# Kernel optimization log

Hardware: AMD Instinct MI355X
Metric: run time of the kernel (lower is better)

Reference implementation:

```python
import jax, jax.numpy as jnp
import numpy as np

NUM_HEADS = 16
KEY_SIZE = 64
D_MODEL = 1024


def setup_inputs() -> dict:
    key = jax.random.key(0)
    ks = jax.random.split(key, 9)
    B, S = 2, 2048
    HK = NUM_HEADS * KEY_SIZE
    s = 1.0 / np.sqrt(D_MODEL)
    return {
        "x": jax.random.normal(ks[0], (B, S, D_MODEL), dtype=jnp.float32),
        "Wq": jax.random.normal(ks[1], (D_MODEL, HK), dtype=jnp.float32) * s,
        "bq": jax.random.normal(ks[2], (HK,), dtype=jnp.float32) * 0.02,
        "Wk": jax.random.normal(ks[3], (D_MODEL, HK), dtype=jnp.float32) * s,
        "bk": jax.random.normal(ks[4], (HK,), dtype=jnp.float32) * 0.02,
        "Wv": jax.random.normal(ks[5], (D_MODEL, HK), dtype=jnp.float32) * s,
        "bv": jax.random.normal(ks[6], (HK,), dtype=jnp.float32) * 0.02,
        "Wo": jax.random.normal(ks[7], (HK, D_MODEL), dtype=jnp.float32) * s,
        "bo": jax.random.normal(ks[8], (D_MODEL,), dtype=jnp.float32) * 0.02,
    }


def reference(x, Wq, bq, Wk, bk, Wv, bv, Wo, bo):
    B, S, _ = x.shape
    H, K = NUM_HEADS, KEY_SIZE
    # QKV projections -> (B, H, S, K)
    def proj(W, b):
        return (x @ W + b).reshape(B, S, H, K).transpose(0, 2, 1, 3)
    q = proj(Wq, bq)
    k = proj(Wk, bk)
    v = proj(Wv, bv)
    scale = jnp.sqrt(jnp.float32(K))
    scores = jnp.einsum('bhsk,bhtk->bhst', q, k) / scale  # (B,H,S,S)
    attn = jax.nn.softmax(scores, axis=-1)
    out = jnp.einsum('bhst,bhtk->bhsk', attn, v)  # (B,H,S,K)
    out = out.transpose(0, 2, 1, 3).reshape(B, S, H * K)
    return out @ Wo + bo
```

## Files before the change

kernel.cpp:

```cpp
#include <hip/hip_runtime.h>


#define NH 16
#define KS 64
#define DM 1024
#define BB 2
#define SS 2048
#define NT (BB*SS)
#define HKD 1024
#define L2E 1.44269504088896340736f

typedef __attribute__((ext_vector_type(4))) float floatx4;
typedef __attribute__((ext_vector_type(8))) short short8;

__device__ __forceinline__ unsigned short f2b(float f) {
  unsigned u = __builtin_bit_cast(unsigned, f);
  u = (u + 0x7fffu + ((u >> 16) & 1u)) >> 16;
  return (unsigned short)u;
}

__device__ __forceinline__ floatx4 mfma16(short8 a, short8 b, floatx4 c) {
  return __builtin_amdgcn_mfma_f32_16x16x32_bf16(a, b, c, 0, 0, 0);
}

__device__ __forceinline__ void async16(const void* g, void* l) {
  __builtin_amdgcn_global_load_lds(
      (const __attribute__((address_space(1))) unsigned int*)g,
      (__attribute__((address_space(3))) unsigned int*)l, 16, 0, 0);
}

__global__ void cast_x_kernel(const float* __restrict__ x, unsigned short* __restrict__ xb) {
  int i = (blockIdx.x * 256 + threadIdx.x) * 4;
  float4 v = *(const float4*)(x + i);
  ushort4 o;
  o.x = f2b(v.x); o.y = f2b(v.y); o.z = f2b(v.z); o.w = f2b(v.w);
  *(ushort4*)(xb + i) = o;
}

__global__ void transw_kernel(const float* __restrict__ Wq, const float* __restrict__ Wk,
                              const float* __restrict__ Wv, const float* __restrict__ Wo,
                              unsigned short* __restrict__ wqt, unsigned short* __restrict__ wkt,
                              unsigned short* __restrict__ wvt, unsigned short* __restrict__ wot) {
  const float* W; unsigned short* Wt;
  if (blockIdx.z == 0)      { W = Wq; Wt = wqt; }
  else if (blockIdx.z == 1) { W = Wk; Wt = wkt; }
  else if (blockIdx.z == 2) { W = Wv; Wt = wvt; }
  else                      { W = Wo; Wt = wot; }
  __shared__ __align__(16) unsigned short tile[64][80];
  int k0 = blockIdx.x * 64, n0 = blockIdx.y * 64;
  int t = threadIdx.x;
  int c0 = (t & 15) * 4, r = t >> 4;
  #pragma unroll
  for (int p = 0; p < 4; ++p) {
    int rr = r + p * 16;
    float4 v = *(const float4*)(W + (k0 + rr) * DM + n0 + c0);
    tile[c0 + 0][rr] = f2b(v.x);
    tile[c0 + 1][rr] = f2b(v.y);
    tile[c0 + 2][rr] = f2b(v.z);
    tile[c0 + 3][rr] = f2b(v.w);
  }
  __syncthreads();
  int cc0 = (t & 7) * 8, rn = t >> 3;
  #pragma unroll
  for (int p = 0; p < 2; ++p) {
    int nn = rn + p * 32;
    *(short8*)(Wt + (n0 + nn) * DM + k0 + cc0) = *(const short8*)(&tile[nn][cc0]);
  }
}

__global__ __launch_bounds__(256) void gemm_qkv_kernel(
    const unsigned short* __restrict__ xb,
    const unsigned short* __restrict__ wqt, const unsigned short* __restrict__ wkt,
    const unsigned short* __restrict__ wvt,
    const float* __restrict__ bq, const float* __restrict__ bk, const float* __restrict__ bv,
    unsigned short* __restrict__ qb, unsigned short* __restrict__ kbuf,
    unsigned short* __restrict__ vbuf) {
  __shared__ __align__(16) unsigned short As[8192], Bs[8192];
  const unsigned short* Bt; const float* bias; unsigned short* dst; float scale;
  if (blockIdx.z == 0)      { Bt = wqt; bias = bq; dst = qb;   scale = 0.125f * L2E; }
  else if (blockIdx.z == 1) { Bt = wkt; bias = bk; dst = kbuf; scale = 1.0f; }
  else                      { Bt = wvt; bias = bv; dst = vbuf; scale = 1.0f; }
  int m0 = blockIdx.x * 128, n0 = blockIdx.y * 128;
  int t = threadIdx.x, w = t >> 6, lane = t & 63, cl = lane & 15, quad = lane >> 4;
  int clm = cl & 7;
  int wr = (w >> 1) * 64, wc = (w & 1) * 64;
  floatx4 acc[4][4];
  #pragma unroll
  for (int i = 0; i < 4; ++i)
    #pragma unroll
    for (int j = 0; j < 4; ++j)
      acc[i][j] = floatx4{0.f, 0.f, 0.f, 0.f};

  for (int kc = 0; kc < DM / 64; ++kc) {
    __syncthreads();
    #pragma unroll
    for (int i = 0; i < 4; ++i) {
      int c = i * 256 + t;
      int row = c >> 3, col8 = (c & 7) ^ (row & 7);
      async16(xb + (m0 + row) * DM + kc * 64 + col8 * 8, &As[c * 8]);
      async16(Bt + (n0 + row) * DM + kc * 64 + col8 * 8, &Bs[c * 8]);
    }
    asm volatile("s_waitcnt vmcnt(0)" ::: "memory");
    __syncthreads();
    #pragma unroll
    for (int kk = 0; kk < 2; ++kk) {
      short8 a[4], b[4];
      #pragma unroll
      for (int i = 0; i < 4; ++i)
        a[i] = *(const short8*)&As[(wr + i * 16 + cl) * 64 + (((kk * 4 + quad) ^ clm) * 8)];
      #pragma unroll
      for (int j = 0; j < 4; ++j)
        b[j] = *(const short8*)&Bs[(wc + j * 16 + cl) * 64 + (((kk * 4 + quad) ^ clm) * 8)];
      #pragma unroll
      for (int i = 0; i < 4; ++i)
        #pragma unroll
        for (int j = 0; j < 4; ++j)
          acc[i][j] = mfma16(a[i], b[j], acc[i][j]);
    }
  }
  int h = (n0 + wc) >> 6;
  #pragma unroll
  for (int j = 0; j < 4; ++j) {
    float bj = bias[n0 + wc + j * 16 + cl];
    int kd = j * 16 + cl;
    #pragma unroll
    for (int i = 0; i < 4; ++i)
      #pragma unroll
      for (int r = 0; r < 4; ++r) {
        int token = m0 + wr + i * 16 + quad * 4 + r;
        int bz = token >> 11, s = token & (SS - 1);
        float val = (acc[i][j][r] + bj) * scale;
        dst[(((bz * NH + h) * SS + s) << 6) + kd] = f2b(val);
      }
  }
}

__global__ void transv_kernel(const unsigned short* __restrict__ v,
                              unsigned short* __restrict__ vt) {
  __shared__ __align__(16) unsigned short tile[64][80];
  int s0 = blockIdx.x * 64, bh = blockIdx.y;
  int t = threadIdx.x;
  int kd0 = (t & 7) * 8, sl = t >> 3;
  #pragma unroll
  for (int p = 0; p < 2; ++p) {
    int sr = sl + p * 32;
    short8 vv = *(const short8*)(v + (bh * SS + s0 + sr) * KS + kd0);
    #pragma unroll
    for (int q = 0; q < 8; ++q) tile[kd0 + q][sr] = ((unsigned short*)&vv)[q];
  }
  __syncthreads();
  int sc0 = (t & 7) * 8, kl = t >> 3;
  #pragma unroll
  for (int p = 0; p < 2; ++p) {
    int kk = kl + p * 32;
    *(short8*)(vt + (bh * KS + kk) * SS + s0 + sc0) = *(const short8*)(&tile[kk][sc0]);
  }
}

__global__ __launch_bounds__(256) void attn_kernel(
    const unsigned short* __restrict__ Q, const unsigned short* __restrict__ Kb,
    const unsigned short* __restrict__ Vt, unsigned short* __restrict__ AO) {
  __shared__ __align__(16) unsigned short Ks[2][4096], Vs[2][4096];
  __shared__ __align__(16) unsigned short Ps[4][1024];
  int t = threadIdx.x, w = t >> 6, lane = t & 63, cl = lane & 15, quad = lane >> 4;
  int clm = cl & 7;
  int h = blockIdx.y, bz = blockIdx.z, bh = bz * NH + h;
  int q0 = blockIdx.x * 64 + w * 16;
  const unsigned short* Qp = Q + (bh * SS + q0) * KS;
  const unsigned short* Kp = Kb + bh * SS * KS;
  const unsigned short* Vp = Vt + bh * KS * SS;
  unsigned short* p_w = Ps[w];

  short8 qa[2];
  #pragma unroll
  for (int c = 0; c < 2; ++c)
    qa[c] = *(const short8*)(Qp + cl * KS + c * 32 + quad * 8);

  float l = 0.f;
  floatx4 oa[4];
  #pragma unroll
  for (int j = 0; j < 4; ++j) oa[j] = floatx4{0.f, 0.f, 0.f, 0.f};

  auto stage = [&](int tile, int buf) {
    const unsigned short* kp = Kp + (tile * 64) * KS;
    #pragma unroll
    for (int i = 0; i < 2; ++i) {
      int c = i * 256 + t;
      int row = c >> 3, col8 = (c & 7) ^ (row & 7);
      async16(kp + row * KS + col8 * 8, &Ks[buf][c * 8]);
    }
    #pragma unroll
    for (int i = 0; i < 2; ++i) {
      int c = i * 256 + t;
      int d = c >> 3, col8 = (c & 7) ^ (d & 7);
      async16(Vp + d * SS + tile * 64 + col8 * 8, &Vs[buf][c * 8]);
    }
  };
  stage(0, 0);
  stage(1, 1);

  const int NTILES = SS / 64;
  for (int it = 0; it < NTILES; ++it) {
    int cur = it & 1;
    if (it < NTILES - 1) asm volatile("s_waitcnt vmcnt(4)" ::: "memory");
    else                 asm volatile("s_waitcnt vmcnt(0)" ::: "memory");
    __syncthreads();

    floatx4 s[4];
    #pragma unroll
    for (int kt = 0; kt < 4; ++kt) {
      short8 kb0 = *(const short8*)&Ks[cur][(kt * 16 + cl) * 64 + ((quad ^ clm) * 8)];
      short8 kb1 = *(const short8*)&Ks[cur][(kt * 16 + cl) * 64 + (((4 + quad) ^ clm) * 8)];
      floatx4 z = {0.f, 0.f, 0.f, 0.f};
      s[kt] = mfma16(kb1, qa[1], mfma16(kb0, qa[0], z));
    }
    #pragma unroll
    for (int kt = 0; kt < 4; ++kt) {
      unsigned u[4];
      #pragma unroll
      for (int r = 0; r < 4; ++r) {
        float p = __builtin_amdgcn_exp2f(s[kt][r]);
        u[r] = __builtin_bit_cast(unsigned, p) & 0xffff0000u;
        l += __builtin_bit_cast(float, u[r]);
      }
      uint2 pk;
      pk.x = (u[0] >> 16) | u[1];
      pk.y = (u[2] >> 16) | u[3];
      int off = cl * 64 + (((kt * 2 + (quad >> 1)) ^ clm) * 8) + (quad & 1) * 4;
      *(uint2*)(p_w + off) = pk;
    }
    asm volatile("s_waitcnt lgkmcnt(0)" ::: "memory");
    short8 pa[2];
    #pragma unroll
    for (int c = 0; c < 2; ++c)
      pa[c] = *(const short8*)(p_w + cl * 64 + (((c * 4 + quad) ^ clm) * 8));
    #pragma unroll
    for (int j = 0; j < 4; ++j) {
      short8 vb0 = *(const short8*)&Vs[cur][(j * 16 + cl) * 64 + ((quad ^ clm) * 8)];
      short8 vb1 = *(const short8*)&Vs[cur][(j * 16 + cl) * 64 + (((4 + quad) ^ clm) * 8)];
      oa[j] = mfma16(vb1, pa[1], mfma16(vb0, pa[0], oa[j]));
    }
    __syncthreads();
    if (it + 2 < NTILES) stage(it + 2, cur);
  }

  l += __shfl_xor(l, 16);
  l += __shfl_xor(l, 32);
  float inv = 1.0f / l;
  unsigned short* aop = AO + (bz * SS + q0 + cl) * DM + h * KS + quad * 4;
  #pragma unroll
  for (int j = 0; j < 4; ++j) {
    unsigned short b0 = f2b(oa[j][0] * inv), b1 = f2b(oa[j][1] * inv);
    unsigned short b2 = f2b(oa[j][2] * inv), b3 = f2b(oa[j][3] * inv);
    uint2 pk;
    pk.x = (unsigned)b0 | ((unsigned)b1 << 16);
    pk.y = (unsigned)b2 | ((unsigned)b3 << 16);
    *(uint2*)(aop + j * 16) = pk;
  }
}

__global__ __launch_bounds__(128) void gemm_out_kernel(
    const unsigned short* __restrict__ ao, const unsigned short* __restrict__ wot,
    const float* __restrict__ bo, float* __restrict__ out) {
  __shared__ __align__(16) unsigned short As[8192], Bs[4096];
  int m0 = blockIdx.x * 128, n0 = blockIdx.y * 64;
  int t = threadIdx.x, w = t >> 6, lane = t & 63, cl = lane & 15, quad = lane >> 4;
  int clm = cl & 7;
  int wr = w * 64;
  floatx4 acc[4][4];
  #pragma unroll
  for (int i = 0; i < 4; ++i)
    #pragma unroll
    for (int j = 0; j < 4; ++j)
      acc[i][j] = floatx4{0.f, 0.f, 0.f, 0.f};

  for (int kc = 0; kc < HKD / 64; ++kc) {
    __syncthreads();
    #pragma unroll
    for (int i = 0; i < 8; ++i) {
      int c = i * 128 + t;
      int row = c >> 3, col8 = (c & 7) ^ (row & 7);
      async16(ao + (m0 + row) * HKD + kc * 64 + col8 * 8, &As[c * 8]);
    }
    #pragma unroll
    for (int i = 0; i < 4; ++i) {
      int c = i * 128 + t;
      int row = c >> 3, col8 = (c & 7) ^ (row & 7);
      async16(wot + (n0 + row) * HKD + kc * 64 + col8 * 8, &Bs[c * 8]);
    }
    asm volatile("s_waitcnt vmcnt(0)" ::: "memory");
    __syncthreads();
    #pragma unroll
    for (int kk = 0; kk < 2; ++kk) {
      short8 a[4], b[4];
      #pragma unroll
      for (int i = 0; i < 4; ++i)
        a[i] = *(const short8*)&As[(wr + i * 16 + cl) * 64 + (((kk * 4 + quad) ^ clm) * 8)];
      #pragma unroll
      for (int j = 0; j < 4; ++j)
        b[j] = *(const short8*)&Bs[(j * 16 + cl) * 64 + (((kk * 4 + quad) ^ clm) * 8)];
      #pragma unroll
      for (int i = 0; i < 4; ++i)
        #pragma unroll
        for (int j = 0; j < 4; ++j)
          acc[i][j] = mfma16(a[i], b[j], acc[i][j]);
    }
  }
  #pragma unroll
  for (int j = 0; j < 4; ++j) {
    float bj = bo[n0 + j * 16 + cl];
    #pragma unroll
    for (int i = 0; i < 4; ++i)
      #pragma unroll
      for (int r = 0; r < 4; ++r) {
        int token = m0 + wr + i * 16 + quad * 4 + r;
        out[token * DM + n0 + j * 16 + cl] = acc[i][j][r] + bj;
      }
  }
}

extern "C" void kernel_launch(void* const* d_in, const int* in_sizes, int n_in,
                              void* d_out, int out_size, void* d_ws, size_t ws_size,
                              hipStream_t stream) {
  const float* x  = (const float*)d_in[0];
  const float* Wq = (const float*)d_in[1];
  const float* bq = (const float*)d_in[2];
  const float* Wk = (const float*)d_in[3];
  const float* bk = (const float*)d_in[4];
  const float* Wv = (const float*)d_in[5];
  const float* bv = (const float*)d_in[6];
  const float* Wo = (const float*)d_in[7];
  const float* bo = (const float*)d_in[8];
  float* out = (float*)d_out;
  char* ws = (char*)d_ws;
  unsigned short* xb  = (unsigned short*)(ws);
  unsigned short* wqt = (unsigned short*)(ws + (8ull  << 20));
  unsigned short* wkt = (unsigned short*)(ws + (10ull << 20));
  unsigned short* wvt = (unsigned short*)(ws + (12ull << 20));
  unsigned short* wot = (unsigned short*)(ws + (14ull << 20));
  unsigned short* qb  = (unsigned short*)(ws + (16ull << 20));
  unsigned short* kbf = (unsigned short*)(ws + (24ull << 20));
  unsigned short* vbf = (unsigned short*)(ws + (32ull << 20));
  unsigned short* vt  = (unsigned short*)(ws + (40ull << 20));
  unsigned short* ao  = (unsigned short*)(ws + (48ull << 20));

  hipLaunchKernelGGL(cast_x_kernel, dim3(NT * DM / 1024), dim3(256), 0, stream, x, xb);
  hipLaunchKernelGGL(transw_kernel, dim3(16, 16, 4), dim3(256), 0, stream,
                     Wq, Wk, Wv, Wo, wqt, wkt, wvt, wot);
  hipLaunchKernelGGL(gemm_qkv_kernel, dim3(NT / 128, HKD / 128, 3), dim3(256), 0, stream,
                     xb, wqt, wkt, wvt, bq, bk, bv, qb, kbf, vbf);
  hipLaunchKernelGGL(transv_kernel, dim3(SS / 64, BB * NH), dim3(256), 0, stream, vbf, vt);
  hipLaunchKernelGGL(attn_kernel, dim3(SS / 64, NH, BB), dim3(256), 0, stream, qb, kbf, vt, ao);
  hipLaunchKernelGGL(gemm_out_kernel, dim3(NT / 128, DM / 64), dim3(128), 0, stream, ao, wot, bo, out);
}
```

Before: 213.5 us.

## Double-buffer GEMM loads and fuse V transpose into QKV epilogue

Both GEMM kernels now use double-buffered 32-wide K tiles, prefetching two stages ahead with partial vmcnt waits so global loads overlap MFMA work. The V projection epilogue transposes its tile through shared memory and writes Vt directly, which removes the separate transv kernel launch and its round trip of V through global memory. The cost is more barriers per K step, since each step now covers half the K width, and a per-wave 9 KB transpose region reused from the staging shared memory.

```diff
diff --git a/kernel.cpp b/kernel.cpp
--- a/kernel.cpp
+++ b/kernel.cpp
@@ -74,15 +74,14 @@
     const unsigned short* __restrict__ wvt,
     const float* __restrict__ bq, const float* __restrict__ bk, const float* __restrict__ bv,
     unsigned short* __restrict__ qb, unsigned short* __restrict__ kbuf,
-    unsigned short* __restrict__ vbuf) {
-  __shared__ __align__(16) unsigned short As[8192], Bs[8192];
-  const unsigned short* Bt; const float* bias; unsigned short* dst; float scale;
-  if (blockIdx.z == 0)      { Bt = wqt; bias = bq; dst = qb;   scale = 0.125f * L2E; }
-  else if (blockIdx.z == 1) { Bt = wkt; bias = bk; dst = kbuf; scale = 1.0f; }
-  else                      { Bt = wvt; bias = bv; dst = vbuf; scale = 1.0f; }
+    unsigned short* __restrict__ vt) {
+  __shared__ __align__(16) unsigned short smem[18432];
+  const unsigned short* Bt; const float* bias; float scale; int zid = blockIdx.z;
+  if (zid == 0)      { Bt = wqt; bias = bq; scale = 0.125f * L2E; }
+  else if (zid == 1) { Bt = wkt; bias = bk; scale = 1.0f; }
+  else               { Bt = wvt; bias = bv; scale = 1.0f; }
   int m0 = blockIdx.x * 128, n0 = blockIdx.y * 128;
   int t = threadIdx.x, w = t >> 6, lane = t & 63, cl = lane & 15, quad = lane >> 4;
-  int clm = cl & 7;
   int wr = (w >> 1) * 64, wc = (w & 1) * 64;
   floatx4 acc[4][4];
   #pragma unroll
@@ -91,69 +90,85 @@
     for (int j = 0; j < 4; ++j)
       acc[i][j] = floatx4{0.f, 0.f, 0.f, 0.f};
 
-  for (int kc = 0; kc < DM / 64; ++kc) {
-    __syncthreads();
-    #pragma unroll
-    for (int i = 0; i < 4; ++i) {
+  auto stage = [&](int kc, int buf) {
+    #pragma unroll
+    for (int i = 0; i < 2; ++i) {
       int c = i * 256 + t;
-      int row = c >> 3, col8 = (c & 7) ^ (row & 7);
-      async16(xb + (m0 + row) * DM + kc * 64 + col8 * 8, &As[c * 8]);
-      async16(Bt + (n0 + row) * DM + kc * 64 + col8 * 8, &Bs[c * 8]);
-    }
-    asm volatile("s_waitcnt vmcnt(0)" ::: "memory");
-    __syncthreads();
-    #pragma unroll
-    for (int kk = 0; kk < 2; ++kk) {
-      short8 a[4], b[4];
-      #pragma unroll
-      for (int i = 0; i < 4; ++i)
-        a[i] = *(const short8*)&As[(wr + i * 16 + cl) * 64 + (((kk * 4 + quad) ^ clm) * 8)];
+      int row = c >> 2, col = (c & 3) ^ (row & 3);
+      async16(xb + (m0 + row) * DM + kc * 32 + col * 8, &smem[buf * 4096 + c * 8]);
+      async16(Bt + (n0 + row) * DM + kc * 32 + col * 8, &smem[8192 + buf * 4096 + c * 8]);
+    }
+  };
+  stage(0, 0);
+  stage(1, 1);
+
+  for (int kc = 0; kc < DM / 32; ++kc) {
+    int cur = kc & 1;
+    if (kc < DM / 32 - 1) asm volatile("s_waitcnt vmcnt(4)" ::: "memory");
+    else                  asm volatile("s_waitcnt vmcnt(0)" ::: "memory");
+    __syncthreads();
+    const unsigned short* Ac = &smem[cur * 4096];
+    const unsigned short* Bc = &smem[8192 + cur * 4096];
+    short8 a[4], b[4];
+    #pragma unroll
+    for (int i = 0; i < 4; ++i)
+      a[i] = *(const short8*)&Ac[(wr + i * 16 + cl) * 32 + ((quad ^ (cl & 3)) * 8)];
+    #pragma unroll
+    for (int j = 0; j < 4; ++j)
+      b[j] = *(const short8*)&Bc[(wc + j * 16 + cl) * 32 + ((quad ^ (cl & 3)) * 8)];
+    #pragma unroll
+    for (int i = 0; i < 4; ++i)
       #pragma unroll
       for (int j = 0; j < 4; ++j)
-        b[j] = *(const short8*)&Bs[(wc + j * 16 + cl) * 64 + (((kk * 4 + quad) ^ clm) * 8)];
+        acc[i][j] = mfma16(a[i], b[j], acc[i][j]);
+    __syncthreads();
+    if (kc + 2 < DM / 32) stage(kc + 2, cur);
+  }
+  __syncthreads();
+
+  int h = (n0 + wc) >> 6;
+  if (zid < 2) {
+    unsigned short* dst = (zid == 0) ? qb : kbuf;
+    #pragma unroll
+    for (int j = 0; j < 4; ++j) {
+      float bj = bias[n0 + wc + j * 16 + cl];
+      int kd = j * 16 + cl;
       #pragma unroll
       for (int i = 0; i < 4; ++i)
         #pragma unroll
-        for (int j = 0; j < 4; ++j)
-          acc[i][j] = mfma16(a[i], b[j], acc[i][j]);
-    }
-  }
-  int h = (n0 + wc) >> 6;
-  #pragma unroll
-  for (int j = 0; j < 4; ++j) {
-    float bj = bias[n0 + wc + j * 16 + cl];
-    int kd = j * 16 + cl;
-    #pragma unroll
-    for (int i = 0; i < 4; ++i)
-      #pragma unroll
-      for (int r = 0; r < 4; ++r) {
-        int token = m0 + wr + i * 16 + quad * 4 + r;
-        int bz = token >> 11, s = token & (SS - 1);
-        float val = (acc[i][j][r] + bj) * scale;
-        dst[(((bz * NH + h) * SS + s) << 6) + kd] = f2b(val);
+        for (int r = 0; r < 4; ++r) {
+          int token = m0 + wr + i * 16 + quad * 4 + r;
+          int bz = token >> 11, s = token & (SS - 1);
+          float val = (acc[i][j][r] + bj) * scale;
+          dst[(((bz * NH + h) * SS + s) << 6) + kd] = f2b(val);
+        }
+    }
+  } else {
+    unsigned short* tr = &smem[w * 4608];
+    #pragma unroll
+    for (int j = 0; j < 4; ++j) {
+      float bj = bias[n0 + wc + j * 16 + cl];
+      #pragma unroll
+      for (int i = 0; i < 4; ++i) {
+        unsigned short b0 = f2b(acc[i][j][0] + bj), b1 = f2b(acc[i][j][1] + bj);
+        unsigned short b2 = f2b(acc[i][j][2] + bj), b3 = f2b(acc[i][j][3] + bj);
+        uint2 pk;
+        pk.x = (unsigned)b0 | ((unsigned)b1 << 16);
+        pk.y = (unsigned)b2 | ((unsigned)b3 << 16);
+        *(uint2*)&tr[(j * 16 + cl) * 72 + i * 16 + quad * 4] = pk;
       }
-  }
-}
-
-__global__ void transv_kernel(const unsigned short* __restrict__ v,
-                              unsigned short* __restrict__ vt) {
-  __shared__ __align__(16) unsigned short tile[64][80];
-  int s0 = blockIdx.x * 64, bh = blockIdx.y;
-  int t = threadIdx.x;
-  int kd0 = (t & 7) * 8, sl = t >> 3;
-  #pragma unroll
-  for (int p = 0; p < 2; ++p) {
-    int sr = sl + p * 32;
-    short8 vv = *(const short8*)(v + (bh * SS + s0 + sr) * KS + kd0);
-    #pragma unroll
-    for (int q = 0; q < 8; ++q) tile[kd0 + q][sr] = ((unsigned short*)&vv)[q];
-  }
-  __syncthreads();
-  int sc0 = (t & 7) * 8, kl = t >> 3;
-  #pragma unroll
-  for (int p = 0; p < 2; ++p) {
-    int kk = kl + p * 32;
-    *(short8*)(vt + (bh * KS + kk) * SS + s0 + sc0) = *(const short8*)(&tile[kk][sc0]);
+    }
+    asm volatile("s_waitcnt lgkmcnt(0)" ::: "memory");
+    int tokbase = m0 + wr;
+    int bz = tokbase >> 11, s0 = tokbase & (SS - 1);
+    unsigned short* vdst = vt + (((bz * NH + h) * KS) * SS) + s0;
+    #pragma unroll
+    for (int p = 0; p < 8; ++p) {
+      int row = p * 8 + (lane >> 3);
+      int tk = (lane & 7) * 8;
+      short8 vv = *(const short8*)&tr[row * 72 + tk];
+      *(short8*)(vdst + row * SS + tk) = vv;
+    }
   }
 }
 
@@ -262,10 +277,9 @@
 __global__ __launch_bounds__(128) void gemm_out_kernel(
     const unsigned short* __restrict__ ao, const unsigned short* __restrict__ wot,
     const float* __restrict__ bo, float* __restrict__ out) {
-  __shared__ __align__(16) unsigned short As[8192], Bs[4096];
+  __shared__ __align__(16) unsigned short As[2][4096], Bs[2][2048];
   int m0 = blockIdx.x * 128, n0 = blockIdx.y * 64;
   int t = threadIdx.x, w = t >> 6, lane = t & 63, cl = lane & 15, quad = lane >> 4;
-  int clm = cl & 7;
   int wr = w * 64;
   floatx4 acc[4][4];
   #pragma unroll
@@ -274,37 +288,42 @@
     for (int j = 0; j < 4; ++j)
       acc[i][j] = floatx4{0.f, 0.f, 0.f, 0.f};
 
-  for (int kc = 0; kc < HKD / 64; ++kc) {
-    __syncthreads();
-    #pragma unroll
-    for (int i = 0; i < 8; ++i) {
-      int c = i * 128 + t;
-      int row = c >> 3, col8 = (c & 7) ^ (row & 7);
-      async16(ao + (m0 + row) * HKD + kc * 64 + col8 * 8, &As[c * 8]);
-    }
+  auto stage = [&](int kc, int buf) {
     #pragma unroll
     for (int i = 0; i < 4; ++i) {
       int c = i * 128 + t;
-      int row = c >> 3, col8 = (c & 7) ^ (row & 7);
-      async16(wot + (n0 + row) * HKD + kc * 64 + col8 * 8, &Bs[c * 8]);
-    }
-    asm volatile("s_waitcnt vmcnt(0)" ::: "memory");
-    __syncthreads();
-    #pragma unroll
-    for (int kk = 0; kk < 2; ++kk) {
-      short8 a[4], b[4];
-      #pragma unroll
-      for (int i = 0; i < 4; ++i)
-        a[i] = *(const short8*)&As[(wr + i * 16 + cl) * 64 + (((kk * 4 + quad) ^ clm) * 8)];
+      int row = c >> 2, col = (c & 3) ^ (row & 3);
+      async16(ao + (m0 + row) * HKD + kc * 32 + col * 8, &As[buf][c * 8]);
+    }
+    #pragma unroll
+    for (int i = 0; i < 2; ++i) {
+      int c = i * 128 + t;
+      int row = c >> 2, col = (c & 3) ^ (row & 3);
+      async16(wot + (n0 + row) * HKD + kc * 32 + col * 8, &Bs[buf][c * 8]);
+    }
+  };
+  stage(0, 0);
+  stage(1, 1);
+
+  for (int kc = 0; kc < HKD / 32; ++kc) {
+    int cur = kc & 1;
+    if (kc < HKD / 32 - 1) asm volatile("s_waitcnt vmcnt(6)" ::: "memory");
+    else                   asm volatile("s_waitcnt vmcnt(0)" ::: "memory");
+    __syncthreads();
+    short8 a[4], b[4];
+    #pragma unroll
+    for (int i = 0; i < 4; ++i)
+      a[i] = *(const short8*)&As[cur][(wr + i * 16 + cl) * 32 + ((quad ^ (cl & 3)) * 8)];
+    #pragma unroll
+    for (int j = 0; j < 4; ++j)
+      b[j] = *(const short8*)&Bs[cur][(j * 16 + cl) * 32 + ((quad ^ (cl & 3)) * 8)];
+    #pragma unroll
+    for (int i = 0; i < 4; ++i)
       #pragma unroll
       for (int j = 0; j < 4; ++j)
-        b[j] = *(const short8*)&Bs[(j * 16 + cl) * 64 + (((kk * 4 + quad) ^ clm) * 8)];
-      #pragma unroll
-      for (int i = 0; i < 4; ++i)
-        #pragma unroll
-        for (int j = 0; j < 4; ++j)
-          acc[i][j] = mfma16(a[i], b[j], acc[i][j]);
-    }
+        acc[i][j] = mfma16(a[i], b[j], acc[i][j]);
+    __syncthreads();
+    if (kc + 2 < HKD / 32) stage(kc + 2, cur);
   }
   #pragma unroll
   for (int j = 0; j < 4; ++j) {
@@ -340,7 +359,6 @@
   unsigned short* wot = (unsigned short*)(ws + (14ull << 20));
   unsigned short* qb  = (unsigned short*)(ws + (16ull << 20));
   unsigned short* kbf = (unsigned short*)(ws + (24ull << 20));
-  unsigned short* vbf = (unsigned short*)(ws + (32ull << 20));
   unsigned short* vt  = (unsigned short*)(ws + (40ull << 20));
   unsigned short* ao  = (unsigned short*)(ws + (48ull << 20));
 
@@ -348,8 +366,7 @@
   hipLaunchKernelGGL(transw_kernel, dim3(16, 16, 4), dim3(256), 0, stream,
                      Wq, Wk, Wv, Wo, wqt, wkt, wvt, wot);
   hipLaunchKernelGGL(gemm_qkv_kernel, dim3(NT / 128, HKD / 128, 3), dim3(256), 0, stream,
-                     xb, wqt, wkt, wvt, bq, bk, bv, qb, kbf, vbf);
-  hipLaunchKernelGGL(transv_kernel, dim3(SS / 64, BB * NH), dim3(256), 0, stream, vbf, vt);
+                     xb, wqt, wkt, wvt, bq, bk, bv, qb, kbf, vt);
   hipLaunchKernelGGL(attn_kernel, dim3(SS / 64, NH, BB), dim3(256), 0, stream, qb, kbf, vt, ao);
   hipLaunchKernelGGL(gemm_out_kernel, dim3(NT / 128, DM / 64), dim3(128), 0, stream, ao, wot, bo, out);
 }
```

Result: no change. 215.3 us (+0.8%).
